# Optimization experiments

Hardware: AMD Instinct MI355X
Metric: run time of the kernel (lower is better)

## Reference

```python
import jax, jax.numpy as jnp
import numpy as np

# mcorrlcorr hyperparameters (closed over as constants; int args to the op)
S = (1, 2)   # stride (sx, sy)
D = (1, 1)   # dilation (dx, dy)
P = (0, 2)   # padding (px, py)
U = (1, 1)   # upsample / input dilation (ux, uy)
R = (0, 0)   # extra output size (rx, ry)


def _out_sizes(nfx, nfy, ngx, ngy):
    sx, sy = S; dx, dy = D; px, py = P; ux, uy = U; rx, ry = R
    # mcorr_valid_size along x, lcorr_valid_size along y (from source)
    nhx = max((ngx + ux - 1) * (px + 1) // (nfx + dx - 1) - sx + 1, 0) + rx
    nhy = max((uy * (ngy - 1) - dy * (nfy - 1) + py) // sy + 1, 0) + ry
    return nhx, nhy


def setup_inputs() -> dict:
    key = jax.random.key(0)
    k1, k2, k3 = jax.random.split(key, 3)
    input = jax.random.normal(k1, (16, 32, 128, 384), dtype=jnp.float32)
    weight = jax.random.normal(k2, (64, 32, 4, 8), dtype=jnp.float32) * 0.05
    bias = jax.random.normal(k3, (64,), dtype=jnp.float32) * 0.05
    return {"input": input, "weight": weight, "bias": bias}


def _mcorrlcorr(input, weight, bias):
    batch, c_in, ngx, ngy = input.shape
    c_out, _, nfx, nfy = weight.shape
    sx, sy = S; dx, dy = D; px, py = P; ux, uy = U
    nhx, nhy = _out_sizes(nfx, nfy, ngx, ngy)
    px1 = px + 1

    # --- multiplicative (Mellin) correlation along x ---
    # gx = (hx+sx)*(fx+dx)/(px+1) - ux  when divisible and in [0, ngx)
    hx = jnp.arange(nhx)
    fxi = jnp.arange(nfx)
    num_x = (hx[:, None] + sx) * (fxi[None, :] + dx)          # [nhx, nfx]
    gx = num_x // px1 - ux
    vx = (num_x % px1 == 0) & (gx >= 0) & (gx < ngx)
    gxc = jnp.clip(gx, 0, ngx - 1)
    # gather along x: G1[b, c, hx, fx, gy_full]
    G1 = input[:, :, gxc, :] * vx.astype(input.dtype)[None, None, :, :, None]

    # contract channels and fx, keep fy separate: U[b, o, hx, fy, ngy]
    Ufy = jnp.einsum('bcxfg,ocfy->boxyg', G1, weight)

    # --- linear correlation along y ---
    # gy = (sy*hy - py + dy*fy)/uy  when divisible and in [0, ngy)
    hy = jnp.arange(nhy)
    fyi = jnp.arange(nfy)
    num_y = sy * hy[:, None] - py + dy * fyi[None, :]          # [nhy, nfy]
    gy = num_y // uy
    vy = (num_y % uy == 0) & (gy >= 0) & (gy < ngy)
    gyc = jnp.clip(gy, 0, ngy - 1)

    def gather_fy(Uf, gyf, vyf):
        # Uf: [b, o, nhx, ngy]; gyf, vyf: [nhy]
        return Uf[..., gyf] * vyf.astype(Uf.dtype)

    # vmap over fy axis (axis 3 of Ufy, axis 1 of gyc/vy) -> [nfy, b, o, nhx, nhy]
    per_fy = jax.vmap(gather_fy, in_axes=(3, 1, 1), out_axes=0)(Ufy, gyc, vy)
    h = per_fy.sum(0) + bias[None, :, None, None]
    return h


def reference(input, weight, bias):
    return _mcorrlcorr(input, weight, bias)
```

## Files before the change

kernel.cpp:

```cpp
#include <hip/hip_runtime.h>
#include <hip/hip_bf16.h>


#define Bb   16
#define NGX  128
#define NGY  384
#define Oo   64
#define NHX  32
#define NHY  190

#define HEAD 4
#define RSX  400
#define XBUF (16 * RSX)

typedef short bf16x8 __attribute__((ext_vector_type(8)));
typedef float f32x4  __attribute__((ext_vector_type(4)));
typedef unsigned short u16x4 __attribute__((ext_vector_type(4)));

__device__ __forceinline__ unsigned short f2bf(float f) {
  __hip_bfloat16 h = __float2bfloat16(f);
  return __builtin_bit_cast(unsigned short, h);
}

__global__ void wprep_kernel(const float* __restrict__ w, unsigned short* __restrict__ wl) {
  int idx = blockIdx.x * 256 + threadIdx.x;
  if (idx >= Oo * 1024) return;
  int k8 = idx >> 9;
  int o  = (idx >> 3) & 63;
  int j  = idx & 7;
  wl[idx] = f2bf(w[o * 1024 + k8 * 8 + j]);
}

__global__ __launch_bounds__(512, 4)
void mcorr_mfma_kernel(const float* __restrict__ in, const unsigned short* __restrict__ wl,
                       const float* __restrict__ bias, float* __restrict__ out) {
  const int tid  = threadIdx.x;
  const int l    = tid & 63;
  const int wv   = tid >> 6;
  const int wo   = wv >> 2;
  const int whq  = wv & 3;
  const int lo16 = l & 15, gq = l >> 4;

  int lid = blockIdx.x + NHX * blockIdx.y;
  int swz = (lid & 7) * 64 + (lid >> 3);
  const int hx = swz & 31;
  const int b  = swz >> 5;

  __shared__ __align__(16) unsigned short xs_[2 * XBUF];

  f32x4 acc[2][3];
  #pragma unroll
  for (int i = 0; i < 2; ++i)
    #pragma unroll
    for (int j = 0; j < 3; ++j) acc[i][j] = (f32x4){0.f, 0.f, 0.f, 0.f};

  {
    int bu = tid >> 8, row = (tid >> 4) & 15, j = tid & 15;
    xs_[bu * XBUF + row * RSX + (j < HEAD ? j : 384 + j)] = 0;
  }

  const int r_st  = tid >> 5;
  const int j0    = tid & 31;
  const int fx_st = r_st & 3;
  const int c_st  = r_st >> 2;
  const int gx_st = (hx + 1) * (fx_st + 1) - 1;
  const float* xbase = in + (((size_t)b * 32 + c_st) * NGX + gx_st) * NGY;
  const size_t cstep = (size_t)4 * NGX * NGY;

  float4 xv[2][3];

#define XLOAD(T) do {                                                    \
    const float* xb_ = xbase + (size_t)(T) * cstep;                      \
    _Pragma("unroll") for (int s_ = 0; s_ < 3; ++s_)                     \
      xv[(T) & 1][s_] = *(const float4*)(xb_ + 4 * j0 + 128 * s_);       \
  } while (0)

#define XCOMMIT(T) do {                                                  \
    unsigned short* row_ = xs_ + ((T) & 1) * XBUF + r_st * RSX;          \
    _Pragma("unroll") for (int s_ = 0; s_ < 3; ++s_) {                   \
      u16x4 h_;                                                          \
      h_[0] = f2bf(xv[(T) & 1][s_].x); h_[1] = f2bf(xv[(T) & 1][s_].y);  \
      h_[2] = f2bf(xv[(T) & 1][s_].z); h_[3] = f2bf(xv[(T) & 1][s_].w);  \
      *(u16x4*)&row_[HEAD + 4 * j0 + 128 * s_] = h_;                     \
    }                                                                    \
  } while (0)

#define BAR() do {                                                       \
    asm volatile("s_waitcnt lgkmcnt(0)" ::: "memory");                   \
    __builtin_amdgcn_s_barrier();                                        \
  } while (0)

#define COMPUTE(T) do {                                                              \
    const unsigned* Xb_ = (const unsigned*)(xs_ + ((T) & 1) * XBUF);                 \
    _Pragma("unroll") for (int cs_ = 0; cs_ < 4; ++cs_) {                            \
      const int r_ = cs_ * 4 + gq;                                                   \
      _Pragma("unroll") for (int tt_ = 0; tt_ < 3; ++tt_) {                          \
        int hy_ = 48 * whq + 16 * tt_ + lo16;                                        \
        const unsigned* xp_ = &Xb_[r_ * 200 + 1 + hy_];                              \
        union { unsigned u[4]; bf16x8 v; } bb_;                                      \
        bb_.u[0] = xp_[0]; bb_.u[1] = xp_[1];                                        \
        bb_.u[2] = xp_[2]; bb_.u[3] = xp_[3];                                        \
        acc[0][tt_] = __builtin_amdgcn_mfma_f32_16x16x32_bf16(                       \
            a_[cs_][0], bb_.v, acc[0][tt_], 0, 0, 0);                                \
        acc[1][tt_] = __builtin_amdgcn_mfma_f32_16x16x32_bf16(                       \
            a_[cs_][1], bb_.v, acc[1][tt_], 0, 0, 0);                                \
      }                                                                              \
    }                                                                                \
  } while (0)

  XLOAD(0);
  XLOAD(1);
  XCOMMIT(0);
  BAR();

  #pragma unroll
  for (int t = 0; t < 8; ++t) {
    bf16x8 a_[4][2];
    #pragma unroll
    for (int cs_ = 0; cs_ < 4; ++cs_) {
      const unsigned short* ap_ =
          wl + ((4 * t + cs_) * 4 + gq) * 512 + (32 * wo + lo16) * 8;
      a_[cs_][0] = *(const bf16x8*)ap_;
      a_[cs_][1] = *(const bf16x8*)(ap_ + 128);
    }
    __builtin_amdgcn_sched_barrier(0);
    if (t < 6) XLOAD(t + 2);
    __builtin_amdgcn_s_setprio(1);
    COMPUTE(t);
    __builtin_amdgcn_s_setprio(0);
    if (t < 7) { XCOMMIT(t + 1); BAR(); }
  }

  #pragma unroll
  for (int mt = 0; mt < 2; ++mt) {
    #pragma unroll
    for (int reg = 0; reg < 4; ++reg) {
      int o = 32 * wo + 16 * mt + 4 * gq + reg;
      float bv = bias[o];
      #pragma unroll
      for (int tt = 0; tt < 3; ++tt) {
        int hy = 48 * whq + 16 * tt + lo16;
        if (hy < NHY)
          out[(((size_t)b * Oo + o) * NHX + hx) * NHY + hy] = acc[mt][tt][reg] + bv;
      }
    }
  }
}

extern "C" void kernel_launch(void* const* d_in, const int* in_sizes, int n_in,
                              void* d_out, int out_size, void* d_ws, size_t ws_size,
                              hipStream_t stream) {
  const float* in   = (const float*)d_in[0];
  const float* w    = (const float*)d_in[1];
  const float* bias = (const float*)d_in[2];
  float* out = (float*)d_out;
  unsigned short* wl = (unsigned short*)d_ws;

  wprep_kernel<<<(Oo * 1024 + 255) / 256, 256, 0, stream>>>(w, wl);

  dim3 grid(NHX, Bb);
  mcorr_mfma_kernel<<<grid, 512, 0, stream>>>(in, wl, bias, out);
}
```

Measured before the change: 33.38 us.

## Give each wave a private LDS input strip to drop block barriers

Each wave now stages only the input columns (plus halo) it needs into its own double-buffered LDS strip, instead of the whole block cooperatively staging full rows. This removes the block-wide barriers between the staging and MFMA phases. In exchange, the two waves sharing a column range load the same global data twice, LDS use per block grows, and the prefetch distance drops from two channel groups to one. The bounds check in the weight prep kernel is also removed.

Measured after the change: 37.20 us. 11.5% more time.

```diff
diff --git a/kernel.cpp b/kernel.cpp
--- a/kernel.cpp
+++ b/kernel.cpp
@@ -9,9 +9,9 @@
 #define NHX  32
 #define NHY  190
 
-#define HEAD 4
-#define RSX  400
-#define XBUF (16 * RSX)
+#define RSW   124
+#define RDW   62
+#define STRIP (16 * RSW)
 
 typedef short bf16x8 __attribute__((ext_vector_type(8)));
 typedef float f32x4  __attribute__((ext_vector_type(4)));
@@ -24,7 +24,6 @@
 
 __global__ void wprep_kernel(const float* __restrict__ w, unsigned short* __restrict__ wl) {
   int idx = blockIdx.x * 256 + threadIdx.x;
-  if (idx >= Oo * 1024) return;
   int k8 = idx >> 9;
   int o  = (idx >> 3) & 63;
   int j  = idx & 7;
@@ -46,7 +45,7 @@
   const int hx = swz & 31;
   const int b  = swz >> 5;
 
-  __shared__ __align__(16) unsigned short xs_[2 * XBUF];
+  __shared__ __align__(16) unsigned short xs_[8 * 2 * STRIP];
 
   f32x4 acc[2][3];
   #pragma unroll
@@ -54,49 +53,55 @@
     #pragma unroll
     for (int j = 0; j < 3; ++j) acc[i][j] = (f32x4){0.f, 0.f, 0.f, 0.f};
 
-  {
-    int bu = tid >> 8, row = (tid >> 4) & 15, j = tid & 15;
-    xs_[bu * XBUF + row * RSX + (j < HEAD ? j : 384 + j)] = 0;
+  unsigned short* wstrip = xs_ + wv * 2 * STRIP;
+
+  const int row  = l >> 2;
+  const int q    = l & 3;
+  const int c_lo = row >> 2;
+  const int fx   = row & 3;
+  const int gx   = (hx + 1) * (fx + 1) - 1;
+  const int sgy  = (whq == 0) ? 0 : 96 * whq - 8;
+  const int nf4  = (whq == 1 || whq == 2) ? 28 : 26;
+  const int d0s  = (whq == 0) ? 8 : 0;
+  const float* src = in + (((size_t)b * 32 + c_lo) * NGX + gx) * NGY + sgy;
+  const size_t cstep = (size_t)4 * NGX * NGY;
+
+  if (whq == 0 || whq == 3) {
+    int zb = (whq == 0) ? 0 : 104;
+    #pragma unroll
+    for (int bu = 0; bu < 2; ++bu)
+      *(unsigned*)&wstrip[bu * STRIP + row * RSW + zb + 2 * q] = 0;
   }
 
-  const int r_st  = tid >> 5;
-  const int j0    = tid & 31;
-  const int fx_st = r_st & 3;
-  const int c_st  = r_st >> 2;
-  const int gx_st = (hx + 1) * (fx_st + 1) - 1;
-  const float* xbase = in + (((size_t)b * 32 + c_st) * NGX + gx_st) * NGY;
-  const size_t cstep = (size_t)4 * NGX * NGY;
+  float4 xv[7];
 
-  float4 xv[2][3];
-
-#define XLOAD(T) do {                                                    \
-    const float* xb_ = xbase + (size_t)(T) * cstep;                      \
-    _Pragma("unroll") for (int s_ = 0; s_ < 3; ++s_)                     \
-      xv[(T) & 1][s_] = *(const float4*)(xb_ + 4 * j0 + 128 * s_);       \
-  } while (0)
-
-#define XCOMMIT(T) do {                                                  \
-    unsigned short* row_ = xs_ + ((T) & 1) * XBUF + r_st * RSX;          \
-    _Pragma("unroll") for (int s_ = 0; s_ < 3; ++s_) {                   \
-      u16x4 h_;                                                          \
-      h_[0] = f2bf(xv[(T) & 1][s_].x); h_[1] = f2bf(xv[(T) & 1][s_].y);  \
-      h_[2] = f2bf(xv[(T) & 1][s_].z); h_[3] = f2bf(xv[(T) & 1][s_].w);  \
-      *(u16x4*)&row_[HEAD + 4 * j0 + 128 * s_] = h_;                     \
+#define WLOAD(T) do {                                                    \
+    const float* s_ = src + (size_t)(T) * cstep;                         \
+    _Pragma("unroll") for (int s2 = 0; s2 < 7; ++s2) {                   \
+      int i4 = q + 4 * s2;                                               \
+      if (i4 < nf4) xv[s2] = *(const float4*)(s_ + 4 * i4);              \
     }                                                                    \
   } while (0)
 
-#define BAR() do {                                                       \
-    asm volatile("s_waitcnt lgkmcnt(0)" ::: "memory");                   \
-    __builtin_amdgcn_s_barrier();                                        \
+#define WCOMMIT(T) do {                                                  \
+    unsigned short* d_ = wstrip + ((T) & 1) * STRIP + row * RSW + d0s;   \
+    _Pragma("unroll") for (int s2 = 0; s2 < 7; ++s2) {                   \
+      int i4 = q + 4 * s2;                                               \
+      if (i4 < nf4) {                                                    \
+        u16x4 h_;                                                        \
+        h_[0] = f2bf(xv[s2].x); h_[1] = f2bf(xv[s2].y);                  \
+        h_[2] = f2bf(xv[s2].z); h_[3] = f2bf(xv[s2].w);                  \
+        *(u16x4*)&d_[4 * i4] = h_;                                       \
+      }                                                                  \
+    }                                                                    \
   } while (0)
 
 #define COMPUTE(T) do {                                                              \
-    const unsigned* Xb_ = (const unsigned*)(xs_ + ((T) & 1) * XBUF);                 \
+    const unsigned* Xb_ = (const unsigned*)(wstrip + ((T) & 1) * STRIP);             \
     _Pragma("unroll") for (int cs_ = 0; cs_ < 4; ++cs_) {                            \
       const int r_ = cs_ * 4 + gq;                                                   \
       _Pragma("unroll") for (int tt_ = 0; tt_ < 3; ++tt_) {                          \
-        int hy_ = 48 * whq + 16 * tt_ + lo16;                                        \
-        const unsigned* xp_ = &Xb_[r_ * 200 + 1 + hy_];                              \
+        const unsigned* xp_ = &Xb_[r_ * RDW + 3 + 16 * tt_ + lo16];                  \
         union { unsigned u[4]; bf16x8 v; } bb_;                                      \
         bb_.u[0] = xp_[0]; bb_.u[1] = xp_[1];                                        \
         bb_.u[2] = xp_[2]; bb_.u[3] = xp_[3];                                        \
@@ -108,10 +113,8 @@
     }                                                                                \
   } while (0)
 
-  XLOAD(0);
-  XLOAD(1);
-  XCOMMIT(0);
-  BAR();
+  WLOAD(0);
+  WCOMMIT(0);
 
   #pragma unroll
   for (int t = 0; t < 8; ++t) {
@@ -124,11 +127,10 @@
       a_[cs_][1] = *(const bf16x8*)(ap_ + 128);
     }
     __builtin_amdgcn_sched_barrier(0);
-    if (t < 6) XLOAD(t + 2);
-    __builtin_amdgcn_s_setprio(1);
+    if (t < 7) WLOAD(t + 1);
+    __builtin_amdgcn_sched_barrier(0);
     COMPUTE(t);
-    __builtin_amdgcn_s_setprio(0);
-    if (t < 7) { XCOMMIT(t + 1); BAR(); }
+    if (t < 7) WCOMMIT(t + 1);
   }
 
   #pragma unroll
@@ -156,7 +158,7 @@
   float* out = (float*)d_out;
   unsigned short* wl = (unsigned short*)d_ws;
 
-  wprep_kernel<<<(Oo * 1024 + 255) / 256, 256, 0, stream>>>(w, wl);
+  wprep_kernel<<<Oo * 1024 / 256, 256, 0, stream>>>(w, wl);
 
   dim3 grid(NHX, Bb);
   mcorr_mfma_kernel<<<grid, 512, 0, stream>>>(in, wl, bias, out);
```
